# Optimization experiments

Hardware: AMD Instinct MI355X
Metric: run time of the kernel (lower is better)

The kernel has to match this reference:

```python
import jax, jax.numpy as jnp
import numpy as np
from jax import lax

FEAT = 56  # features_size
SR = 2     # sr_ratio
NUM_HEADS = 8

# Constant relative-distance indices, shape (N, N, 2) with values in [0, 2*FEAT-2]
_idx = np.array([[i, j] for i in range(FEAT) for j in range(FEAT)])
REL = jnp.asarray(_idx[None, :, :] - _idx[:, None, :] + FEAT - 1)  # (N, N, 2)


def setup_inputs() -> dict:
    key = jax.random.key(0)
    ks = jax.random.split(key, 8)
    dim = 256
    B = 4
    x = jax.random.normal(ks[0], (B, dim, FEAT, FEAT), dtype=jnp.float32)
    Wq = jax.random.normal(ks[1], (dim, dim), dtype=jnp.float32) * 0.02
    Wkv = jax.random.normal(ks[2], (dim, 2 * dim), dtype=jnp.float32) * 0.02
    sr_w = jax.random.normal(ks[3], (dim, dim, SR, SR), dtype=jnp.float32) * 0.02  # OIHW
    sr_b = jnp.zeros((dim,), dtype=jnp.float32)
    ln_g = jnp.ones((dim,), dtype=jnp.float32)
    ln_b = jnp.zeros((dim,), dtype=jnp.float32)
    pos_emb = jax.random.normal(ks[4], (2 * FEAT - 1, 2 * FEAT - 1), dtype=jnp.float32) * 0.2
    proj_w = jax.random.normal(ks[5], (dim, dim), dtype=jnp.float32) * 0.02
    proj_b = jnp.zeros((dim,), dtype=jnp.float32)
    return {"x": x, "Wq": Wq, "Wkv": Wkv, "sr_w": sr_w, "sr_b": sr_b,
            "ln_g": ln_g, "ln_b": ln_b, "pos_emb": pos_emb,
            "proj_w": proj_w, "proj_b": proj_b}


def reference(x, Wq, Wkv, sr_w, sr_b, ln_g, ln_b, pos_emb, proj_w, proj_b):
    B, C, H, W = x.shape
    N = H * W
    h = NUM_HEADS
    hd = C // h
    scale = hd ** -0.5

    x_q = x.reshape(B, C, N).transpose(0, 2, 1)            # (B, N, C)
    q = (x_q @ Wq).reshape(B, N, h, hd).transpose(0, 2, 1, 3)  # (B, h, N, hd)

    # spatial reduction conv (kernel=stride=SR) + layernorm
    xr = lax.conv_general_dilated(x, sr_w, (SR, SR), 'VALID',
                                  dimension_numbers=('NCHW', 'OIHW', 'NCHW'))
    xr = xr + sr_b[None, :, None, None]
    Nk = (H // SR) * (W // SR)
    x_kv = xr.reshape(B, C, Nk).transpose(0, 2, 1)          # (B, Nk, C)
    mu = jnp.mean(x_kv, axis=-1, keepdims=True)
    var = jnp.var(x_kv, axis=-1, keepdims=True)
    x_kv = (x_kv - mu) * lax.rsqrt(var + 1e-5) * ln_g + ln_b

    # kv projection; einops '(dim h l)' split: head_dim slowest, l fastest
    kv = (x_kv @ Wkv).reshape(B, Nk, hd, h, 2)
    k = kv[..., 0].transpose(0, 3, 1, 2)                    # (B, h, Nk, hd)
    v = kv[..., 1].transpose(0, 3, 1, 2)                    # (B, h, Nk, hd)

    attn = jnp.einsum('bhnd,bhmd->bhnm', q, k) * scale      # (B, h, N, Nk)
    bias = pos_emb[REL[..., 0], REL[..., 1]][:, :Nk]        # (N, Nk)
    attn = jax.nn.softmax(attn + bias, axis=-1)

    out = jnp.einsum('bhnm,bhmd->bhnd', attn, v)            # (B, h, N, hd)
    out = out.transpose(0, 2, 1, 3).reshape(B, N, C)
    out = out @ proj_w + proj_b
    return out.transpose(0, 2, 1).reshape(B, C, H, W)
```

## Files before the change

kernel.cpp:

```cpp
#include <hip/hip_runtime.h>
#include <hip/hip_bf16.h>

typedef float f32x4 __attribute__((ext_vector_type(4)));
typedef short s16x8 __attribute__((ext_vector_type(8)));
typedef unsigned short u16x4 __attribute__((ext_vector_type(4)));
typedef unsigned short u16x8 __attribute__((ext_vector_type(8)));

#define MFMA16(a,b,c) __builtin_amdgcn_mfma_f32_16x16x32_bf16(a,b,c,0,0,0)

#define NTOK 3136
#define NKV  784
#define NKVP 800
#define CD   256
#define NH   8
#define HD   32
#define PEW  111
#define LOG2E 1.4426950408889634f
#define SC2  (0.17677669529663687f * 1.4426950408889634f)

static __device__ __forceinline__ unsigned short f2b(float f){
  unsigned int u = __float_as_uint(f);
  return (unsigned short)((u + 0x7fffu + ((u>>16)&1u)) >> 16);
}
static __device__ __forceinline__ unsigned short f2b_fast(float f){
  __hip_bfloat16 h = __float2bfloat16(f);
  return *reinterpret_cast<unsigned short*>(&h);
}
static __device__ __forceinline__ float b2f(unsigned short u){
  return __uint_as_float(((unsigned int)u)<<16);
}
static __device__ __forceinline__ void gload16(const unsigned short* g, unsigned short* l){
  __builtin_amdgcn_global_load_lds(
      (const __attribute__((address_space(1))) unsigned int*)g,
      (__attribute__((address_space(3))) unsigned int*)l, 16, 0, 0);
}

__global__ __launch_bounds__(256) void k_prep(
      const float* __restrict__ Wq, const float* __restrict__ Wkv,
      const float* __restrict__ pw, const float* __restrict__ srw,
      const float* __restrict__ pos, const float* __restrict__ x,
      unsigned short* __restrict__ WqT, unsigned short* __restrict__ WkvT,
      unsigned short* __restrict__ pwT, unsigned short* __restrict__ srwb2,
      unsigned short* __restrict__ bias2, unsigned short* __restrict__ xbf,
      unsigned short* __restrict__ kb, unsigned short* __restrict__ vT){
  __shared__ float tile[64][65];
  const int blk = blockIdx.x, t = threadIdx.x;
  if (blk < 2048){
    int i = blk*256 + t;
    if (i < 65536){ int nn=i>>8, kk=i&255; WqT[i] = f2b(Wq[kk*256+nn]); }
    else if (i < 196608){ int j=i-65536; int c2=j>>8, kk=j&255; WkvT[j] = f2b(Wkv[kk*512+c2]); }
    else if (i < 262144){ int j=i-196608; int cc=j>>8, kk=j&255; pwT[j] = f2b(pw[kk*256+cc]); }
    else { int j=i-262144; int o=j>>10, rem=j&1023, khw=rem>>8, ci=rem&255;
           srwb2[j] = f2b(srw[o*1024 + ci*4 + khw]); }
  } else if (blk < 2176){
    int i = (blk-2048)*256 + t;
    if (i < 16384){
      int bh=i>>9, r=i&511, ridx=r>>5, d=r&31;
      int row = 776 + (ridx&7) + (ridx>>3)*16;
      kb[((size_t)bh*NKVP + row)*HD + d] = 0;
    } else {
      int j=i-16384;
      int bh=j>>9, r=j&511, d=r>>4, key=784+(r&15);
      vT[((size_t)bh*HD + d)*NKVP + key] = 0;
    }
  } else if (blk < 5312){
    int n = blk - 2176;
    if (t < 200){
      int nr = (n*9363)>>19, nc = n - nr*56;
      u16x4 o;
#pragma unroll
      for (int j=0;j<4;++j){
        int key = t*4 + j;
        float v;
        if (key < NKV){
          int tt = (key*9363)>>19, mm = key - tt*56;
          v = pos[(tt-nr+55)*PEW + (mm-nc+55)] * LOG2E;
        } else v = -100000.f;
        o[j] = f2b(v);
      }
      *(u16x4*)&bias2[(size_t)n*NKVP + t*4] = o;
    }
  } else {
    int bx = blk - 5312;
    const int n0 = (bx%49)*64; int c4 = bx/49;
    const int c0 = (c4&3)*64, b = c4>>2;
    const int tx = t&15, ty = t>>4;
#pragma unroll
    for (int j=0;j<4;++j){
      f32x4 v = *(const f32x4*)&x[(size_t)(b*CD + c0+ty+j*16)*NTOK + n0 + tx*4];
      tile[ty+j*16][tx*4+0]=v[0]; tile[ty+j*16][tx*4+1]=v[1];
      tile[ty+j*16][tx*4+2]=v[2]; tile[ty+j*16][tx*4+3]=v[3];
    }
    __syncthreads();
    const int nr = t>>2, ccb = (t&3)*16;
    u16x8 o0, o1;
#pragma unroll
    for (int u=0;u<8;++u){ o0[u] = f2b(tile[ccb+u][nr]); o1[u] = f2b(tile[ccb+8+u][nr]); }
    unsigned short* dst = &xbf[((size_t)b*NTOK + n0+nr)*CD + c0 + ccb];
    *(u16x8*)dst = o0;
    *(u16x8*)(dst+8) = o1;
  }
}

__global__ __launch_bounds__(256) void k_qproj(const unsigned short* __restrict__ xbf,
      const unsigned short* __restrict__ WqT, unsigned short* __restrict__ qb){
  const int tid=threadIdx.x, wv=tid>>6, l=tid&63, g=l>>4, ln16=l&15;
  const int bI = blockIdx.x/49;
  const int n0 = (blockIdx.x%49)*64;
  const int m0 = n0 + (wv>>1)*32;
  const int c0 = blockIdx.y*64 + (wv&1)*32;
  const unsigned short* ap0 = &xbf[((size_t)bI*NTOK + m0+ln16)*CD + g*8];
  const unsigned short* ap1 = ap0 + 16*CD;
  const unsigned short* bp0 = &WqT[(size_t)(c0+ln16)*CD + g*8];
  const unsigned short* bp1 = bp0 + 16*CD;
  f32x4 acc[2][2] = {};
  s16x8 a0 = *(const s16x8*)ap0, a1 = *(const s16x8*)ap1;
  s16x8 w0 = *(const s16x8*)bp0, w1 = *(const s16x8*)bp1;
#pragma unroll
  for (int k0=0; k0<CD; k0+=32){
    s16x8 na0 = *(const s16x8*)(ap0 + k0+32);
    s16x8 na1 = *(const s16x8*)(ap1 + k0+32);
    s16x8 nw0 = *(const s16x8*)(bp0 + k0+32);
    s16x8 nw1 = *(const s16x8*)(bp1 + k0+32);
    acc[0][0] = MFMA16(a0, w0, acc[0][0]);
    acc[0][1] = MFMA16(a0, w1, acc[0][1]);
    acc[1][0] = MFMA16(a1, w0, acc[1][0]);
    acc[1][1] = MFMA16(a1, w1, acc[1][1]);
    a0=na0; a1=na1; w0=nw0; w1=nw1;
  }
#pragma unroll
  for (int mi=0;mi<2;++mi)
#pragma unroll
    for (int ni=0;ni<2;++ni){
      int c = c0 + ni*16 + ln16;
#pragma unroll
      for (int r=0;r<4;++r){
        int n = m0 + mi*16 + g*4 + r;
        qb[((size_t)bI*NTOK + n)*CD + c] = f2b(acc[mi][ni][r] * SC2);
      }
    }
}

__global__ __launch_bounds__(256) void k_conv(const unsigned short* __restrict__ xbf,
      const unsigned short* __restrict__ srwb2, const float* __restrict__ srb,
      float* __restrict__ convo){
  const int tid=threadIdx.x, wv=tid>>6, l=tid&63, g=l>>4, ln16=l&15;
  const int m0 = blockIdx.x*64 + (wv>>1)*32;
  const int c0 = blockIdx.y*64 + (wv&1)*32;
  size_t abase[2][4];
#pragma unroll
  for (int mi=0;mi<2;++mi){
    int m = m0 + mi*16 + ln16;
    int bb = (m>=2352)?3:(m>=1568)?2:(m>=784)?1:0;
    int nk = m - bb*784;
    int pp = (nk*9363)>>18, qq = nk - pp*28;
#pragma unroll
    for (int khw=0;khw<4;++khw){
      int kh = khw>>1, kw = khw&1;
      abase[mi][khw] = ((size_t)bb*NTOK + (2*pp+kh)*56 + 2*qq+kw)*CD;
    }
  }
  const unsigned short* wp0 = &srwb2[(size_t)(c0+ln16)*1024 + g*8];
  const unsigned short* wp1 = wp0 + 16*1024;
  f32x4 acc[2][2] = {};
  s16x8 a0 = *(const s16x8*)&xbf[abase[0][0] + g*8];
  s16x8 a1 = *(const s16x8*)&xbf[abase[1][0] + g*8];
  s16x8 w0 = *(const s16x8*)wp0;
  s16x8 w1 = *(const s16x8*)wp1;
#pragma unroll
  for (int s=0; s<32; ++s){
    const int s1 = s+1;
    const int khw2 = (s1>>3)&3, kc2 = (s1&7)*32;
    const int woff = (s1&31)*32;
    s16x8 na0 = *(const s16x8*)&xbf[abase[0][khw2] + kc2 + g*8];
    s16x8 na1 = *(const s16x8*)&xbf[abase[1][khw2] + kc2 + g*8];
    s16x8 nw0 = *(const s16x8*)(wp0 + woff);
    s16x8 nw1 = *(const s16x8*)(wp1 + woff);
    acc[0][0] = MFMA16(a0, w0, acc[0][0]);
    acc[0][1] = MFMA16(a0, w1, acc[0][1]);
    acc[1][0] = MFMA16(a1, w0, acc[1][0]);
    acc[1][1] = MFMA16(a1, w1, acc[1][1]);
    a0=na0; a1=na1; w0=nw0; w1=nw1;
  }
#pragma unroll
  for (int mi=0;mi<2;++mi)
#pragma unroll
    for (int ni=0;ni<2;++ni){
      int c = c0 + ni*16 + ln16;
      float bias = srb[c];
#pragma unroll
      for (int r=0;r<4;++r){
        int m = m0 + mi*16 + g*4 + r;
        convo[(size_t)m*CD + c] = acc[mi][ni][r] + bias;
      }
    }
}

__global__ void k_ln(const float* __restrict__ co, const float* __restrict__ gam,
                     const float* __restrict__ bet, unsigned short* __restrict__ kvbf){
  const int row = blockIdx.x, t = threadIdx.x;
  float v = co[(size_t)row*CD + t];
  float s = v, s2 = v*v;
#pragma unroll
  for (int o=32; o>0; o>>=1){ s += __shfl_down(s,o); s2 += __shfl_down(s2,o); }
  __shared__ float ps[4], ps2[4];
  int wid = t>>6, lane = t&63;
  if (lane==0){ ps[wid]=s; ps2[wid]=s2; }
  __syncthreads();
  if (t==0){
    float a = ps[0]+ps[1]+ps[2]+ps[3];
    float a2 = ps2[0]+ps2[1]+ps2[2]+ps2[3];
    float mu = a*(1.f/CD);
    float var = a2*(1.f/CD) - mu*mu;
    ps[0] = mu; ps2[0] = rsqrtf(var + 1e-5f);
  }
  __syncthreads();
  float mu = ps[0], rs = ps2[0];
  kvbf[(size_t)row*CD + t] = f2b((v-mu)*rs*gam[t] + bet[t]);
}

__global__ __launch_bounds__(256) void k_kv(const unsigned short* __restrict__ kvbf,
      const unsigned short* __restrict__ WkvT, unsigned short* __restrict__ kb,
      unsigned short* __restrict__ vT){
  const int tid=threadIdx.x, wv=tid>>6, l=tid&63, g=l>>4, ln16=l&15;
  const int m0 = blockIdx.x*64 + (wv>>1)*32;
  const int c0 = blockIdx.y*64 + (wv&1)*32;
  const unsigned short* ap0 = &kvbf[(size_t)(m0+ln16)*CD + g*8];
  const unsigned short* ap1 = ap0 + 16*CD;
  const unsigned short* bp0 = &WkvT[(size_t)(c0+ln16)*CD + g*8];
  const unsigned short* bp1 = bp0 + 16*CD;
  f32x4 acc[2][2] = {};
  s16x8 a0 = *(const s16x8*)ap0, a1 = *(const s16x8*)ap1;
  s16x8 w0 = *(const s16x8*)bp0, w1 = *(const s16x8*)bp1;
#pragma unroll
  for (int k0=0; k0<CD; k0+=32){
    s16x8 na0 = *(const s16x8*)(ap0 + k0+32);
    s16x8 na1 = *(const s16x8*)(ap1 + k0+32);
    s16x8 nw0 = *(const s16x8*)(bp0 + k0+32);
    s16x8 nw1 = *(const s16x8*)(bp1 + k0+32);
    acc[0][0] = MFMA16(a0, w0, acc[0][0]);
    acc[0][1] = MFMA16(a0, w1, acc[0][1]);
    acc[1][0] = MFMA16(a1, w0, acc[1][0]);
    acc[1][1] = MFMA16(a1, w1, acc[1][1]);
    a0=na0; a1=na1; w0=nw0; w1=nw1;
  }
#pragma unroll
  for (int mi=0;mi<2;++mi)
#pragma unroll
    for (int ni=0;ni<2;++ni){
      int c2 = c0 + ni*16 + ln16;
      int d = c2>>4, hh = (c2>>1)&7;
#pragma unroll
      for (int r=0;r<4;++r){
        int m = m0 + mi*16 + g*4 + r;
        int bq = (m>=2352)?3:(m>=1568)?2:(m>=784)?1:0;
        int nk = m - bq*784;
        unsigned short val = f2b(acc[mi][ni][r]);
        if (c2&1){
          vT[(((size_t)bq*NH+hh)*HD + d)*NKVP + nk] = val;
        } else {
          int chunk = nk & ~31, pos = nk & 31;
          int gg = pos>>3, jj = pos&7;
          int row = (jj<4) ? (gg*4+jj) : (16 + gg*4 + (jj-4));
          kb[(((size_t)bq*NH+hh)*NKVP + chunk + row)*HD + d] = val;
        }
      }
    }
}

__global__ __launch_bounds__(256) void k_attn(const unsigned short* __restrict__ qb,
      const unsigned short* __restrict__ kb, const unsigned short* __restrict__ vT,
      const unsigned short* __restrict__ bias2, unsigned short* __restrict__ aout){
  __shared__ unsigned short kv[2][2048];
  const int tid=threadIdx.x, wv=tid>>6, l=tid&63, g=l>>4, ln16=l&15;
  const int bh = blockIdx.x, b = bh>>3, h = bh&7;
  const int nw = blockIdx.y*64 + wv*16;
  const s16x8 qf = *(const s16x8*)&qb[((size_t)b*NTOK + nw + ln16)*CD + h*HD + g*8];
  const unsigned short* kbase = kb + (size_t)bh*NKVP*HD;
  const unsigned short* vbase = vT + (size_t)bh*HD*NKVP;
  const unsigned short* bp = bias2 + (size_t)(nw + ln16)*NKVP + g*8;
  const unsigned short* sp = (wv < 2)
      ? (kbase + wv*512 + l*8)
      : (vbase + (size_t)((wv&1)*16 + (l>>2))*NKVP + (l&3)*8);
  const int sstep = (wv < 2) ? 1024 : 32;
  unsigned short* ldst0 = &kv[0][wv*512];
  unsigned short* ldst1 = &kv[1][wv*512];
  f32x4 accO0 = {}, accO1 = {};
  float S = 0.f;
  const f32x4 zf = {};
  gload16(sp, ldst0);
  u16x8 bb = *(const u16x8*)bp;
  __syncthreads();
  int cur = 0;
  for (int it=0; it<25; ++it){
    u16x8 nbb = bb;
    if (it < 24){
      gload16(sp + (it+1)*sstep, cur ? ldst0 : ldst1);
      nbb = *(const u16x8*)(bp + (it+1)*32);
    }
    __builtin_amdgcn_sched_barrier(0);
    const unsigned short* kc = kv[cur];
    s16x8 ka0 = *(const s16x8*)&kc[ln16*32 + g*8];
    s16x8 ka1 = *(const s16x8*)&kc[512 + ln16*32 + g*8];
    s16x8 v0  = *(const s16x8*)&kc[1024 + ln16*32 + g*8];
    s16x8 v1  = *(const s16x8*)&kc[1536 + ln16*32 + g*8];
    f32x4 d0 = MFMA16(ka0, qf, zf);
    f32x4 d1 = MFMA16(ka1, qf, zf);
    float p[8];
#pragma unroll
    for (int r=0;r<4;++r){
      p[r]   = exp2f(d0[r] + b2f(bb[r]));
      p[4+r] = exp2f(d1[r] + b2f(bb[4+r]));
    }
    S += ((p[0]+p[1])+(p[2]+p[3])) + ((p[4]+p[5])+(p[6]+p[7]));
    s16x8 pf;
#pragma unroll
    for (int j=0;j<8;++j) pf[j] = (short)f2b_fast(p[j]);
    accO0 = MFMA16(pf, v0, accO0);
    accO1 = MFMA16(pf, v1, accO1);
    __syncthreads();
    cur ^= 1; bb = nbb;
  }
  S += __shfl_xor(S, 16);
  S += __shfl_xor(S, 32);
#pragma unroll
  for (int r=0;r<4;++r){
    float Sr = __shfl(S, g*4 + r);
    float inv = 1.f / Sr;
    int n = nw + g*4 + r;
    aout[((size_t)b*NTOK + n)*CD + h*HD + ln16]      = f2b(accO0[r]*inv);
    aout[((size_t)b*NTOK + n)*CD + h*HD + 16 + ln16] = f2b(accO1[r]*inv);
  }
}

__global__ __launch_bounds__(256) void k_proj(const unsigned short* __restrict__ ain,
      const unsigned short* __restrict__ pwT, const float* __restrict__ pb,
      float* __restrict__ out){
  const int tid=threadIdx.x, wv=tid>>6, l=tid&63, g=l>>4, ln16=l&15;
  const int bI = blockIdx.x/49;
  const int n0 = (blockIdx.x%49)*64;
  const int nsub = n0 + (wv&1)*32;
  const int c0 = blockIdx.y*64 + (wv>>1)*32;
  const unsigned short* ap0 = &pwT[(size_t)(c0+ln16)*CD + g*8];
  const unsigned short* ap1 = ap0 + 16*CD;
  const unsigned short* bp0 = &ain[((size_t)bI*NTOK + nsub+ln16)*CD + g*8];
  const unsigned short* bp1 = bp0 + 16*CD;
  f32x4 acc[2][2] = {};
  s16x8 a0 = *(const s16x8*)ap0, a1 = *(const s16x8*)ap1;
  s16x8 w0 = *(const s16x8*)bp0, w1 = *(const s16x8*)bp1;
#pragma unroll
  for (int k0=0; k0<CD; k0+=32){
    s16x8 na0 = *(const s16x8*)(ap0 + k0+32);
    s16x8 na1 = *(const s16x8*)(ap1 + k0+32);
    s16x8 nw0 = *(const s16x8*)(bp0 + k0+32);
    s16x8 nw1 = *(const s16x8*)(bp1 + k0+32);
    acc[0][0] = MFMA16(a0, w0, acc[0][0]);
    acc[0][1] = MFMA16(a0, w1, acc[0][1]);
    acc[1][0] = MFMA16(a1, w0, acc[1][0]);
    acc[1][1] = MFMA16(a1, w1, acc[1][1]);
    a0=na0; a1=na1; w0=nw0; w1=nw1;
  }
#pragma unroll
  for (int mi=0;mi<2;++mi)
#pragma unroll
    for (int r=0;r<4;++r){
      int c = c0 + mi*16 + g*4 + r;
      float bias = pb[c];
#pragma unroll
      for (int ni=0;ni<2;++ni){
        int n = nsub + ni*16 + ln16;
        out[((size_t)bI*CD + c)*NTOK + n] = acc[mi][ni][r] + bias;
      }
    }
}

extern "C" void kernel_launch(void* const* d_in, const int* in_sizes, int n_in,
                              void* d_out, int out_size, void* d_ws, size_t ws_size,
                              hipStream_t stream){
  const float* x   = (const float*)d_in[0];
  const float* Wq  = (const float*)d_in[1];
  const float* Wkv = (const float*)d_in[2];
  const float* srw = (const float*)d_in[3];
  const float* srb = (const float*)d_in[4];
  const float* lng = (const float*)d_in[5];
  const float* lnb = (const float*)d_in[6];
  const float* pos = (const float*)d_in[7];
  const float* pw  = (const float*)d_in[8];
  const float* pb  = (const float*)d_in[9];
  float* out = (float*)d_out;

  unsigned char* p = (unsigned char*)d_ws;
  unsigned short* WqT   = (unsigned short*)(p + 0);
  unsigned short* WkvT  = (unsigned short*)(p + 131072);
  unsigned short* pwT   = (unsigned short*)(p + 393216);
  unsigned short* srwb2 = (unsigned short*)(p + 524288);
  unsigned short* bias2 = (unsigned short*)(p + 1048576);
  unsigned short* xbf   = (unsigned short*)(p + 6066176);
  unsigned short* qbuf  = (unsigned short*)(p + 12488704);
  float*          convo = (float*)        (p + 18911232);
  unsigned short* kvbf  = (unsigned short*)(p + 22122496);
  unsigned short* kbuf  = (unsigned short*)(p + 23728128);
  unsigned short* vT    = (unsigned short*)(p + 25366528);
  unsigned short* aout  = (unsigned short*)(p + 27004928);

  k_prep <<<6096, 256, 0, stream>>>(Wq, Wkv, pw, srw, pos, x,
                                    WqT, WkvT, pwT, srwb2, bias2, xbf, kbuf, vT);
  k_qproj<<<dim3(196,4), 256, 0, stream>>>(xbf, WqT, qbuf);
  k_conv <<<dim3(49,4),  256, 0, stream>>>(xbf, srwb2, srb, convo);
  k_ln   <<<3136, 256, 0, stream>>>(convo, lng, lnb, kvbf);
  k_kv   <<<dim3(49,8),  256, 0, stream>>>(kvbf, WkvT, kbuf, vT);
  k_attn <<<dim3(32,49), 256, 0, stream>>>(qbuf, kbuf, vT, bias2, aout);
  k_proj <<<dim3(196,4), 256, 0, stream>>>(aout, pwT, pb, out);
}
```

Before: 198.2 us.

## Triple-buffer attention K/V tiles with XOR-swizzled LDS and manual waitcnt

Replaces the double-buffered K/V shared-memory pipeline in the attention kernel with a three-stage ring, prefetching two tiles ahead and using explicit vmcnt waits plus a single barrier per iteration instead of two syncthreads. K/V rows are stored with an XOR swizzle to reduce LDS bank conflicts on the fragment reads, and the MFMA section is raised in priority with s_setprio. This aims to hide global-load latency and reduce sync overhead, at the cost of more LDS per block and reliance on the vmcnt count matching the number of outstanding loads (including the bias loads).

```diff
diff --git a/kernel.cpp b/kernel.cpp
--- a/kernel.cpp
+++ b/kernel.cpp
@@ -271,7 +271,7 @@
 __global__ __launch_bounds__(256) void k_attn(const unsigned short* __restrict__ qb,
       const unsigned short* __restrict__ kb, const unsigned short* __restrict__ vT,
       const unsigned short* __restrict__ bias2, unsigned short* __restrict__ aout){
-  __shared__ unsigned short kv[2][2048];
+  __shared__ unsigned short kv0[2048], kv1[2048], kv2[2048];
   const int tid=threadIdx.x, wv=tid>>6, l=tid&63, g=l>>4, ln16=l&15;
   const int bh = blockIdx.x, b = bh>>3, h = bh&7;
   const int nw = blockIdx.y*64 + wv*16;
@@ -279,31 +279,35 @@
   const unsigned short* kbase = kb + (size_t)bh*NKVP*HD;
   const unsigned short* vbase = vT + (size_t)bh*HD*NKVP;
   const unsigned short* bp = bias2 + (size_t)(nw + ln16)*NKVP + g*8;
+  const int lslot = ((l&3)^((l>>3)&3))*8;
   const unsigned short* sp = (wv < 2)
-      ? (kbase + wv*512 + l*8)
-      : (vbase + (size_t)((wv&1)*16 + (l>>2))*NKVP + (l&3)*8);
+      ? (kbase + (size_t)(wv*16 + (l>>2))*HD + lslot)
+      : (vbase + (size_t)((wv-2)*16 + (l>>2))*NKVP + lslot);
   const int sstep = (wv < 2) ? 1024 : 32;
-  unsigned short* ldst0 = &kv[0][wv*512];
-  unsigned short* ldst1 = &kv[1][wv*512];
+  const int ko0 = ln16*32 + (g ^ ((ln16>>1)&3))*8;
+  unsigned short *bA = kv0, *bB = kv1, *bC = kv2;
   f32x4 accO0 = {}, accO1 = {};
   float S = 0.f;
   const f32x4 zf = {};
-  gload16(sp, ldst0);
+  gload16(sp,          bA + wv*512);
   u16x8 bb = *(const u16x8*)bp;
-  __syncthreads();
-  int cur = 0;
+  gload16(sp + sstep,  bB + wv*512);
+  u16x8 b1 = *(const u16x8*)(bp + 32);
   for (int it=0; it<25; ++it){
-    u16x8 nbb = bb;
-    if (it < 24){
-      gload16(sp + (it+1)*sstep, cur ? ldst0 : ldst1);
-      nbb = *(const u16x8*)(bp + (it+1)*32);
-    }
+    if (it < 23) asm volatile("s_waitcnt vmcnt(2)" ::: "memory");
+    else         asm volatile("s_waitcnt vmcnt(0)" ::: "memory");
+    __builtin_amdgcn_s_barrier();
     __builtin_amdgcn_sched_barrier(0);
-    const unsigned short* kc = kv[cur];
-    s16x8 ka0 = *(const s16x8*)&kc[ln16*32 + g*8];
-    s16x8 ka1 = *(const s16x8*)&kc[512 + ln16*32 + g*8];
-    s16x8 v0  = *(const s16x8*)&kc[1024 + ln16*32 + g*8];
-    s16x8 v1  = *(const s16x8*)&kc[1536 + ln16*32 + g*8];
+    u16x8 b2 = b1;
+    if (it < 23){
+      gload16(sp + (it+2)*sstep, bC + wv*512);
+      b2 = *(const u16x8*)(bp + (it+2)*32);
+    }
+    s16x8 ka0 = *(const s16x8*)&bA[ko0];
+    s16x8 ka1 = *(const s16x8*)&bA[512 + ko0];
+    s16x8 v0  = *(const s16x8*)&bA[1024 + ko0];
+    s16x8 v1  = *(const s16x8*)&bA[1536 + ko0];
+    __builtin_amdgcn_s_setprio(1);
     f32x4 d0 = MFMA16(ka0, qf, zf);
     f32x4 d1 = MFMA16(ka1, qf, zf);
     float p[8];
@@ -318,8 +322,9 @@
     for (int j=0;j<8;++j) pf[j] = (short)f2b_fast(p[j]);
     accO0 = MFMA16(pf, v0, accO0);
     accO1 = MFMA16(pf, v1, accO1);
-    __syncthreads();
-    cur ^= 1; bb = nbb;
+    __builtin_amdgcn_s_setprio(0);
+    unsigned short* tmp = bA; bA = bB; bB = bC; bC = tmp;
+    bb = b1; b1 = b2;
   }
   S += __shfl_xor(S, 16);
   S += __shfl_xor(S, 32);
```

After: 193.4 us. -2.4%, faster.
